# Kernel tuning notes

Measured on AMD Instinct MI355X. Metric: run time of the kernel, lower is better.

## Reference

```python
import jax, jax.numpy as jnp
import numpy as np
from jax import lax

STORAGE = 8
HIDDEN_HEAD = 32
N_BLOCKS = 16


def _conv(x, w, b, padding):
    # x: NCHW, w: OIHW
    y = lax.conv_general_dilated(
        x, w, window_strides=(1, 1), padding=padding,
        dimension_numbers=("NCHW", "OIHW", "NCHW"))
    return y + b[None, :, None, None]


def _min_pool3(x):
    # 3x3 sliding-window min, stride 1, same padding (pad value +inf so it
    return lax.reduce_window(x, float("inf"), lax.min,
                             (1, 1, 3, 3), (1, 1, 1, 1), "SAME")


def setup_inputs() -> dict:
    key = jax.random.key(0)
    ks = jax.random.split(key, 7)
    B, H, W = 8, 512, 512
    x = jax.random.normal(ks[0], (B, 1, H, W), dtype=jnp.float32)
    # initial 1x1 conv: 1 -> 8
    w0 = jax.random.normal(ks[1], (STORAGE, 1, 1, 1), dtype=jnp.float32) * 1.0
    b0 = jax.random.normal(ks[2], (STORAGE,), dtype=jnp.float32) * 0.1
    # head conv 3x3: 8 -> 32
    w1 = jax.random.normal(ks[3], (HIDDEN_HEAD, STORAGE, 3, 3), dtype=jnp.float32) * (1.0 / np.sqrt(STORAGE * 9))
    b1 = jax.random.normal(ks[4], (HIDDEN_HEAD,), dtype=jnp.float32) * 0.1
    # head conv 1x1: 32 -> 1
    w2 = jax.random.normal(ks[5], (1, HIDDEN_HEAD, 1, 1), dtype=jnp.float32) * (1.0 / np.sqrt(HIDDEN_HEAD))
    b2 = jax.random.normal(ks[6], (1,), dtype=jnp.float32) * 0.1
    return {"x": x, "w0": w0, "b0": b0, "w1": w1, "b1": b1, "w2": w2, "b2": b2}


def reference(x, w0, b0, w1, b1, w2, b2):
    h = _conv(x, w0, b0, "SAME")  # [B,8,H,W]
    for _ in range(N_BLOCKS):
        h = h + _min_pool3(h)
    h = _conv(h, w1, b1, "SAME")  # [B,32,H,W]
    h = jax.nn.relu(h)
    return _conv(h, w2, b2, "SAME")  # [B,1,H,W]
```

## Files before the change

### kernel.cpp

```cpp
#include <hip/hip_runtime.h>
#include <math.h>


#define N_PIX (512*512)
#define INF __builtin_inff()

typedef __attribute__((ext_vector_type(2))) float f2;

__device__ __forceinline__ float dpp_shr1(float v, float fill) {
    return __int_as_float(__builtin_amdgcn_update_dpp(
        __float_as_int(fill), __float_as_int(v), 0x138, 0xF, 0xF, false));
}
__device__ __forceinline__ float dpp_shl1(float v, float fill) {
    return __int_as_float(__builtin_amdgcn_update_dpp(
        __float_as_int(fill), __float_as_int(v), 0x130, 0xF, 0xF, false));
}
__device__ __forceinline__ float vmin3(float a, float b, float c) {
    float d;
    asm("v_min3_f32 %0, %1, %2, %3" : "=v"(d) : "v"(a), "v"(b), "v"(c));
    return d;
}

struct Row8 { float4 a, b; };

__device__ __forceinline__ Row8 row_update8(const Row8 up, const Row8 mid, const Row8 dn)
{
    float v0 = vmin3(up.a.x, mid.a.x, dn.a.x);
    float v1 = vmin3(up.a.y, mid.a.y, dn.a.y);
    float v2 = vmin3(up.a.z, mid.a.z, dn.a.z);
    float v3 = vmin3(up.a.w, mid.a.w, dn.a.w);
    float v4 = vmin3(up.b.x, mid.b.x, dn.b.x);
    float v5 = vmin3(up.b.y, mid.b.y, dn.b.y);
    float v6 = vmin3(up.b.z, mid.b.z, dn.b.z);
    float v7 = vmin3(up.b.w, mid.b.w, dn.b.w);
    float vmL = dpp_shr1(v7, INF);
    float vmR = dpp_shl1(v0, INF);
    Row8 o;
    o.a.x = mid.a.x + vmin3(vmL, v0, v1);
    o.a.y = mid.a.y + vmin3(v0, v1, v2);
    o.a.z = mid.a.z + vmin3(v1, v2, v3);
    o.a.w = mid.a.w + vmin3(v2, v3, v4);
    o.b.x = mid.b.x + vmin3(v3, v4, v5);
    o.b.y = mid.b.y + vmin3(v4, v5, v6);
    o.b.z = mid.b.z + vmin3(v5, v6, v7);
    o.b.w = mid.b.w + vmin3(v6, v7, vmR);
    return o;
}

__device__ __forceinline__ void halo_write(float* hp, const Row8& v) {
    hp[0*64]=v.a.x; hp[1*64]=v.a.y; hp[2*64]=v.a.z; hp[3*64]=v.a.w;
    hp[4*64]=v.b.x; hp[5*64]=v.b.y; hp[6*64]=v.b.z; hp[7*64]=v.b.w;
}
__device__ __forceinline__ Row8 halo_read(const float* hp) {
    Row8 v;
    v.a.x=hp[0*64]; v.a.y=hp[1*64]; v.a.z=hp[2*64]; v.a.w=hp[3*64];
    v.b.x=hp[4*64]; v.b.y=hp[5*64]; v.b.z=hp[6*64]; v.b.w=hp[7*64];
    return v;
}

__global__ __launch_bounds__(512, 2) void erode16_kernel(
    const float* __restrict__ x, float* __restrict__ A,
    const float* __restrict__ w0, const float* __restrict__ b0,
    const float* __restrict__ w1, const float* __restrict__ b1,
    float* __restrict__ W)
{
    if (blockIdx.x == 0 && blockIdx.y == 0 && threadIdx.x < 288) {
        int tid = threadIdx.x;
        int oc = tid / 9, k = tid - oc*9;
        float wp = 0.f, wq = 0.f;
        for (int ic = 0; ic < 8; ++ic) {
            float a = w0[ic];
            float w = w1[oc*72 + ic*9 + k];
            if (a > 0.f) wp += w * a;
            else         wq += w * (-a);
        }
        W[(oc*9 + k)*2 + 0] = wp;
        W[(oc*9 + k)*2 + 1] = wq;
        if (k == 0) {
            float beta[9];
            for (int kk = 0; kk < 9; ++kk) {
                float s = 0.f;
                for (int ic = 0; ic < 8; ++ic) s += b0[ic] * w1[oc*72 + ic*9 + kk];
                beta[kk] = 65536.0f * s;
            }
            float R[3], Lb[3], Rr[3];
            for (int r = 0; r < 3; ++r) {
                R[r]  = beta[r*3] + beta[r*3+1] + beta[r*3+2];
                Lb[r] = beta[r*3 + 0];
                Rr[r] = beta[r*3 + 2];
            }
            float bb = b1[oc];
            float Dv[3]  = { bb + R[1] + R[2], bb + R[0] + R[1] + R[2], bb + R[0] + R[1] };
            float ELv[3] = { Lb[1] + Lb[2], Lb[0] + Lb[1] + Lb[2], Lb[0] + Lb[1] };
            float ERv[3] = { Rr[1] + Rr[2], Rr[0] + Rr[1] + Rr[2], Rr[0] + Rr[1] };
            for (int c = 0; c < 3; ++c) {
                W[576 + (c*32 + oc)*2 + 0] = 0.5f * Dv[c];
                W[576 + (c*32 + oc)*2 + 1] = 0.5f * Dv[c];
                W[768 + c*32 + oc] = ELv[c];
                W[864 + c*32 + oc] = ERv[c];
            }
        }
    }

    __shared__ float halo[2][8][4][8][64];
    const int tid   = threadIdx.x;
    const int lane  = tid & 63;
    const int w     = tid >> 6;
    const int ty    = blockIdx.x;
    const int plane = blockIdx.y;
    const int colg  = lane * 8;
    const int row0g = ty*32 - 16 + w*8;

    const int wS = __builtin_amdgcn_readfirstlane(w);
    const bool edge_band = (wS == 0) || (wS == 7);

    const float* sp = x + (plane & 7)*N_PIX;
    const float sgn = (plane >= 8) ? -1.f : 1.f;

    Row8 h[8];
    #pragma unroll
    for (int r = 0; r < 8; ++r) {
        int gy = row0g + r;
        if ((unsigned)gy < 512u) {
            const float* rp = sp + gy*512 + colg;
            float4 a = *(const float4*)rp;
            float4 b = *(const float4*)(rp + 4);
            h[r].a = make_float4(a.x*sgn, a.y*sgn, a.z*sgn, a.w*sgn);
            h[r].b = make_float4(b.x*sgn, b.y*sgn, b.z*sgn, b.w*sgn);
        } else {
            h[r].a = make_float4(INF, INF, INF, INF);
            h[r].b = h[r].a;
        }
    }

    const Row8 inf8 = { make_float4(INF,INF,INF,INF), make_float4(INF,INF,INF,INF) };
    for (int s = 0; s < 8; ++s) {
        int par = s & 1;
        if (edge_band && s >= 4) { __syncthreads(); continue; }
        halo_write(&halo[par][w][0][0][lane], h[0]);
        halo_write(&halo[par][w][1][0][lane], h[1]);
        halo_write(&halo[par][w][2][0][lane], h[6]);
        halo_write(&halo[par][w][3][0][lane], h[7]);
        Row8 n2 = row_update8(h[1], h[2], h[3]);
        Row8 n3 = row_update8(h[2], h[3], h[4]);
        Row8 n4 = row_update8(h[3], h[4], h[5]);
        Row8 n5 = row_update8(h[4], h[5], h[6]);
        __syncthreads();
        Row8 um2 = inf8, um1 = inf8, dp0 = inf8, dp1 = inf8;
        if (w > 0) {
            um2 = halo_read(&halo[par][w-1][2][0][lane]);
            um1 = halo_read(&halo[par][w-1][3][0][lane]);
        }
        if (w < 7) {
            dp0 = halo_read(&halo[par][w+1][0][0][lane]);
            dp1 = halo_read(&halo[par][w+1][1][0][lane]);
        }
        Row8 nm1 = row_update8(um2, um1, h[0]);
        Row8 n0  = row_update8(um1, h[0], h[1]);
        Row8 n1  = row_update8(h[0], h[1], h[2]);
        Row8 n6  = row_update8(h[5], h[6], h[7]);
        Row8 n7  = row_update8(h[6], h[7], dp0);
        Row8 n8  = row_update8(h[7], dp0, dp1);
        h[0] = row_update8(nm1, n0, n1);
        h[1] = row_update8(n0,  n1, n2);
        h[2] = row_update8(n1,  n2, n3);
        h[3] = row_update8(n2,  n3, n4);
        h[4] = row_update8(n3,  n4, n5);
        h[5] = row_update8(n4,  n5, n6);
        h[6] = row_update8(n5,  n6, n7);
        h[7] = row_update8(n6,  n7, n8);
    }

    if (w >= 2 && w <= 5) {
        float* dp = A + plane*N_PIX;
        #pragma unroll
        for (int r = 0; r < 8; ++r) {
            float* op = dp + (row0g + r)*512 + colg;
            *(float4*)op       = h[r].a;
            *(float4*)(op + 4) = h[r].b;
        }
    }
}

__global__ __launch_bounds__(256) void head_kernel(
    const float* __restrict__ A, const float* __restrict__ W,
    const float* __restrict__ w2, const float* __restrict__ b2,
    float* __restrict__ out)
{
    const int tid  = threadIdx.x;
    const int lane = tid & 63;
    const int w    = tid >> 6;
    const int img  = blockIdx.x >> 7;
    const int y    = (blockIdx.x & 127)*4 + w;
    const int x0   = lane*8;

    const float* P = A + img*N_PIX;
    const float* Q = A + (8 + img)*N_PIX;

    f2 pq[3][10];
    #pragma unroll
    for (int dy = 0; dy < 3; ++dy) {
        int gy = y + dy - 1;
        if ((unsigned)gy < 512u) {
            const float* rp = P + gy*512 + x0;
            const float* rq = Q + gy*512 + x0;
            float4 a = *(const float4*)rp;
            float4 b = *(const float4*)(rp + 4);
            float4 c = *(const float4*)rq;
            float4 d = *(const float4*)(rq + 4);
            pq[dy][1] = (f2){a.x, c.x}; pq[dy][2] = (f2){a.y, c.y};
            pq[dy][3] = (f2){a.z, c.z}; pq[dy][4] = (f2){a.w, c.w};
            pq[dy][5] = (f2){b.x, d.x}; pq[dy][6] = (f2){b.y, d.y};
            pq[dy][7] = (f2){b.z, d.z}; pq[dy][8] = (f2){b.w, d.w};
            pq[dy][0] = (f2){dpp_shr1(b.w, 0.f), dpp_shr1(d.w, 0.f)};
            pq[dy][9] = (f2){dpp_shl1(a.x, 0.f), dpp_shl1(c.x, 0.f)};
        } else {
            #pragma unroll
            for (int j = 0; j < 10; ++j) pq[dy][j] = (f2){0.f, 0.f};
        }
    }

    const int wcase = (y == 0) ? 0 : ((y == 511) ? 2 : 1);
    const f2*    DH  = (const f2*)(W + 576);
    const float* ELt = W + 768 + wcase*32;
    const float* ERt = W + 864 + wcase*32;
    const float  mL  = (lane == 0)  ? -1.f : 0.f;
    const float  mR  = (lane == 63) ? -1.f : 0.f;

    float o[8];
    #pragma unroll
    for (int j = 0; j < 8; ++j) o[j] = 0.f;

    const f2* Wv = (const f2*)W;
    #pragma unroll 2
    for (int oc = 0; oc < 32; ++oc) {
        f2 acc[8];
        {
            f2 wv0 = Wv[oc*9];
            f2 hb  = DH[wcase*32 + oc];
            #pragma unroll
            for (int j = 0; j < 8; ++j) acc[j] = wv0 * pq[0][j] + hb;
        }
        #pragma unroll
        for (int t = 1; t < 9; ++t) {
            const int ky = t / 3, kx = t - ky*3;
            f2 wv = Wv[oc*9 + t];
            #pragma unroll
            for (int j = 0; j < 8; ++j) acc[j] += wv * pq[ky][kx + j];
        }
        float cl = ELt[oc];
        float cr = ERt[oc];
        float s[8];
        #pragma unroll
        for (int j = 0; j < 8; ++j) s[j] = acc[j].x + acc[j].y;
        s[0] = fmaf(cl, mL, s[0]);
        s[7] = fmaf(cr, mR, s[7]);
        float sc = w2[oc];
        #pragma unroll
        for (int j = 0; j < 8; ++j) o[j] += fmaxf(s[j], 0.f) * sc;
    }

    float bb = b2[0];
    float* op = out + img*N_PIX + y*512 + x0;
    *(float4*)(op)     = make_float4(o[0]+bb, o[1]+bb, o[2]+bb, o[3]+bb);
    *(float4*)(op + 4) = make_float4(o[4]+bb, o[5]+bb, o[6]+bb, o[7]+bb);
}

extern "C" void kernel_launch(void* const* d_in, const int* in_sizes, int n_in,
                              void* d_out, int out_size, void* d_ws, size_t ws_size,
                              hipStream_t stream) {
    const float* x  = (const float*)d_in[0];
    const float* w0 = (const float*)d_in[1];
    const float* b0 = (const float*)d_in[2];
    const float* w1 = (const float*)d_in[3];
    const float* b1 = (const float*)d_in[4];
    const float* w2 = (const float*)d_in[5];
    const float* b2 = (const float*)d_in[6];
    float* out = (float*)d_out;

    float* wsf = (float*)d_ws;
    float* A = wsf;
    float* W = wsf + 16*N_PIX;

    dim3 eg(16, 16);
    erode16_kernel<<<eg, 512, 0, stream>>>(x, A, w0, b0, w1, b1, W);

    head_kernel<<<1024, 256, 0, stream>>>(A, W, w2, b2, out);
}
```

Measured before the change: 122.7 us.

## Pack two output channels per pk_fma in head and vectorize swizzled LDS halo

The head conv is reorganized so each packed f32 lane holds two output channels rather than the P/Q halves of one channel. Weights are stored as scalar pairs and fed through inline v_pk_fma with op_sel, which removes the per-channel horizontal add and halves the epilogue relu/scale work. The erosion halo buffer moves from strided scalar LDS accesses to float4 accesses with an XOR swizzle to limit bank conflicts. The cost is more pk_fma issues, since the P and Q passes now run separately, and the use of inline asm with SGPR operands that the compiler must materialize.

Result: no change. 122.8 us (+0.1%).

```diff
diff --git a/kernel.cpp b/kernel.cpp
--- a/kernel.cpp
+++ b/kernel.cpp
@@ -6,6 +6,13 @@
 #define INF __builtin_inff()
 
 typedef __attribute__((ext_vector_type(2))) float f2;
+
+__device__ __forceinline__ unsigned long long f2bits(f2 v) {
+    union { f2 f; unsigned long long u; } c; c.f = v; return c.u;
+}
+__device__ __forceinline__ f2 bits2f(unsigned long long u) {
+    union { f2 f; unsigned long long u; } c; c.u = u; return c.f;
+}
 
 __device__ __forceinline__ float dpp_shr1(float v, float fill) {
     return __int_as_float(__builtin_amdgcn_update_dpp(
@@ -19,6 +26,25 @@
     float d;
     asm("v_min3_f32 %0, %1, %2, %3" : "=v"(d) : "v"(a), "v"(b), "v"(c));
     return d;
+}
+
+__device__ __forceinline__ void pkfma_P(f2& acc, unsigned long long w, f2 pq) {
+    unsigned long long a = f2bits(acc), p = f2bits(pq);
+    asm("v_pk_fma_f32 %0, %1, %2, %0 op_sel:[0,0,0] op_sel_hi:[1,0,1]"
+        : "+v"(a) : "s"(w), "v"(p));
+    acc = bits2f(a);
+}
+__device__ __forceinline__ void pkfma_Q(f2& acc, unsigned long long w, f2 pq) {
+    unsigned long long a = f2bits(acc), p = f2bits(pq);
+    asm("v_pk_fma_f32 %0, %1, %2, %0 op_sel:[0,1,0] op_sel_hi:[1,1,1]"
+        : "+v"(a) : "s"(w), "v"(p));
+    acc = bits2f(a);
+}
+__device__ __forceinline__ void pkmul_P(f2& acc, unsigned long long w, f2 pq) {
+    unsigned long long a, p = f2bits(pq);
+    asm("v_pk_mul_f32 %0, %1, %2 op_sel:[0,0] op_sel_hi:[1,0]"
+        : "=v"(a) : "s"(w), "v"(p));
+    acc = bits2f(a);
 }
 
 struct Row8 { float4 a, b; };
@@ -47,14 +73,14 @@
     return o;
 }
 
-__device__ __forceinline__ void halo_write(float* hp, const Row8& v) {
-    hp[0*64]=v.a.x; hp[1*64]=v.a.y; hp[2*64]=v.a.z; hp[3*64]=v.a.w;
-    hp[4*64]=v.b.x; hp[5*64]=v.b.y; hp[6*64]=v.b.z; hp[7*64]=v.b.w;
-}
-__device__ __forceinline__ Row8 halo_read(const float* hp) {
+__device__ __forceinline__ void halo_write(float* hp, int f0, int f1, const Row8& v) {
+    *(float4*)(hp + f0) = v.a;
+    *(float4*)(hp + f1) = v.b;
+}
+__device__ __forceinline__ Row8 halo_read(const float* hp, int f0, int f1) {
     Row8 v;
-    v.a.x=hp[0*64]; v.a.y=hp[1*64]; v.a.z=hp[2*64]; v.a.w=hp[3*64];
-    v.b.x=hp[4*64]; v.b.y=hp[5*64]; v.b.z=hp[6*64]; v.b.w=hp[7*64];
+    v.a = *(const float4*)(hp + f0);
+    v.b = *(const float4*)(hp + f1);
     return v;
 }
 
@@ -62,11 +88,12 @@
     const float* __restrict__ x, float* __restrict__ A,
     const float* __restrict__ w0, const float* __restrict__ b0,
     const float* __restrict__ w1, const float* __restrict__ b1,
-    float* __restrict__ W)
+    const float* __restrict__ w2, float* __restrict__ W)
 {
     if (blockIdx.x == 0 && blockIdx.y == 0 && threadIdx.x < 288) {
         int tid = threadIdx.x;
         int oc = tid / 9, k = tid - oc*9;
+        int o = oc >> 1, hf = oc & 1;
         float wp = 0.f, wq = 0.f;
         for (int ic = 0; ic < 8; ++ic) {
             float a = w0[ic];
@@ -74,8 +101,8 @@
             if (a > 0.f) wp += w * a;
             else         wq += w * (-a);
         }
-        W[(oc*9 + k)*2 + 0] = wp;
-        W[(oc*9 + k)*2 + 1] = wq;
+        W[(o*9 + k)*2 + hf]       = wp;
+        W[288 + (o*9 + k)*2 + hf] = wq;
         if (k == 0) {
             float beta[9];
             for (int kk = 0; kk < 9; ++kk) {
@@ -94,15 +121,15 @@
             float ELv[3] = { Lb[1] + Lb[2], Lb[0] + Lb[1] + Lb[2], Lb[0] + Lb[1] };
             float ERv[3] = { Rr[1] + Rr[2], Rr[0] + Rr[1] + Rr[2], Rr[0] + Rr[1] };
             for (int c = 0; c < 3; ++c) {
-                W[576 + (c*32 + oc)*2 + 0] = 0.5f * Dv[c];
-                W[576 + (c*32 + oc)*2 + 1] = 0.5f * Dv[c];
-                W[768 + c*32 + oc] = ELv[c];
-                W[864 + c*32 + oc] = ERv[c];
+                W[576 + c*32 + o*2 + hf] = Dv[c];
+                W[672 + c*32 + o*2 + hf] = ELv[c];
+                W[768 + c*32 + o*2 + hf] = ERv[c];
             }
-        }
-    }
-
-    __shared__ float halo[2][8][4][8][64];
+            W[864 + o*2 + hf] = w2[oc];
+        }
+    }
+
+    __shared__ float halo[2][8][4][512];
     const int tid   = threadIdx.x;
     const int lane  = tid & 63;
     const int w     = tid >> 6;
@@ -110,6 +137,9 @@
     const int plane = blockIdx.y;
     const int colg  = lane * 8;
     const int row0g = ty*32 - 16 + w*8;
+
+    const int f0 = (lane*8)     ^ (lane & 4);
+    const int f1 = (lane*8 + 4) ^ (lane & 4);
 
     const int wS = __builtin_amdgcn_readfirstlane(w);
     const bool edge_band = (wS == 0) || (wS == 7);
@@ -137,10 +167,10 @@
     for (int s = 0; s < 8; ++s) {
         int par = s & 1;
         if (edge_band && s >= 4) { __syncthreads(); continue; }
-        halo_write(&halo[par][w][0][0][lane], h[0]);
-        halo_write(&halo[par][w][1][0][lane], h[1]);
-        halo_write(&halo[par][w][2][0][lane], h[6]);
-        halo_write(&halo[par][w][3][0][lane], h[7]);
+        halo_write(&halo[par][w][0][0], f0, f1, h[0]);
+        halo_write(&halo[par][w][1][0], f0, f1, h[1]);
+        halo_write(&halo[par][w][2][0], f0, f1, h[6]);
+        halo_write(&halo[par][w][3][0], f0, f1, h[7]);
         Row8 n2 = row_update8(h[1], h[2], h[3]);
         Row8 n3 = row_update8(h[2], h[3], h[4]);
         Row8 n4 = row_update8(h[3], h[4], h[5]);
@@ -148,12 +178,12 @@
         __syncthreads();
         Row8 um2 = inf8, um1 = inf8, dp0 = inf8, dp1 = inf8;
         if (w > 0) {
-            um2 = halo_read(&halo[par][w-1][2][0][lane]);
-            um1 = halo_read(&halo[par][w-1][3][0][lane]);
+            um2 = halo_read(&halo[par][w-1][2][0], f0, f1);
+            um1 = halo_read(&halo[par][w-1][3][0], f0, f1);
         }
         if (w < 7) {
-            dp0 = halo_read(&halo[par][w+1][0][0][lane]);
-            dp1 = halo_read(&halo[par][w+1][1][0][lane]);
+            dp0 = halo_read(&halo[par][w+1][0][0], f0, f1);
+            dp1 = halo_read(&halo[par][w+1][1][0], f0, f1);
         }
         Row8 nm1 = row_update8(um2, um1, h[0]);
         Row8 n0  = row_update8(um1, h[0], h[1]);
@@ -184,8 +214,7 @@
 
 __global__ __launch_bounds__(256) void head_kernel(
     const float* __restrict__ A, const float* __restrict__ W,
-    const float* __restrict__ w2, const float* __restrict__ b2,
-    float* __restrict__ out)
+    const float* __restrict__ b2, float* __restrict__ out)
 {
     const int tid  = threadIdx.x;
     const int lane = tid & 63;
@@ -221,49 +250,65 @@
     }
 
     const int wcase = (y == 0) ? 0 : ((y == 511) ? 2 : 1);
-    const f2*    DH  = (const f2*)(W + 576);
-    const float* ELt = W + 768 + wcase*32;
-    const float* ERt = W + 864 + wcase*32;
-    const float  mL  = (lane == 0)  ? -1.f : 0.f;
-    const float  mR  = (lane == 63) ? -1.f : 0.f;
-
-    float o[8];
+    const unsigned long long* WPv = (const unsigned long long*)W;
+    const unsigned long long* WQv = (const unsigned long long*)(W + 288);
+    const f2* Dpv  = (const f2*)(W + 576 + wcase*32);
+    const f2* ELv  = (const f2*)(W + 672 + wcase*32);
+    const f2* ERv  = (const f2*)(W + 768 + wcase*32);
+    const f2* w2v  = (const f2*)(W + 864);
+    const float mLs = (lane == 0)  ? -1.f : 0.f;
+    const float mRs = (lane == 63) ? -1.f : 0.f;
+    const f2 mLp = (f2){mLs, mLs};
+    const f2 mRp = (f2){mRs, mRs};
+
+    f2 opk[8];
     #pragma unroll
-    for (int j = 0; j < 8; ++j) o[j] = 0.f;
-
-    const f2* Wv = (const f2*)W;
+    for (int j = 0; j < 8; ++j) opk[j] = (f2){0.f, 0.f};
+
     #pragma unroll 2
-    for (int oc = 0; oc < 32; ++oc) {
+    for (int o = 0; o < 16; ++o) {
         f2 acc[8];
         {
-            f2 wv0 = Wv[oc*9];
-            f2 hb  = DH[wcase*32 + oc];
+            unsigned long long wv = WPv[o*9];
             #pragma unroll
-            for (int j = 0; j < 8; ++j) acc[j] = wv0 * pq[0][j] + hb;
+            for (int j = 0; j < 8; ++j) pkmul_P(acc[j], wv, pq[0][j]);
         }
         #pragma unroll
         for (int t = 1; t < 9; ++t) {
             const int ky = t / 3, kx = t - ky*3;
-            f2 wv = Wv[oc*9 + t];
+            unsigned long long wv = WPv[o*9 + t];
             #pragma unroll
-            for (int j = 0; j < 8; ++j) acc[j] += wv * pq[ky][kx + j];
-        }
-        float cl = ELt[oc];
-        float cr = ERt[oc];
-        float s[8];
-        #pragma unroll
-        for (int j = 0; j < 8; ++j) s[j] = acc[j].x + acc[j].y;
-        s[0] = fmaf(cl, mL, s[0]);
-        s[7] = fmaf(cr, mR, s[7]);
-        float sc = w2[oc];
-        #pragma unroll
-        for (int j = 0; j < 8; ++j) o[j] += fmaxf(s[j], 0.f) * sc;
+            for (int j = 0; j < 8; ++j) pkfma_P(acc[j], wv, pq[ky][kx + j]);
+        }
+        #pragma unroll
+        for (int t = 0; t < 9; ++t) {
+            const int ky = t / 3, kx = t - ky*3;
+            unsigned long long wv = WQv[o*9 + t];
+            #pragma unroll
+            for (int j = 0; j < 8; ++j) pkfma_Q(acc[j], wv, pq[ky][kx + j]);
+        }
+        f2 bp = Dpv[o];
+        #pragma unroll
+        for (int j = 0; j < 8; ++j) acc[j] += bp;
+        acc[0] += ELv[o] * mLp;
+        acc[7] += ERv[o] * mRp;
+        f2 sc = w2v[o];
+        #pragma unroll
+        for (int j = 0; j < 8; ++j) {
+            acc[j].x = fmaxf(acc[j].x, 0.f);
+            acc[j].y = fmaxf(acc[j].y, 0.f);
+            opk[j] += acc[j] * sc;
+        }
     }
 
     float bb = b2[0];
+    float o0 = opk[0].x + opk[0].y + bb, o1 = opk[1].x + opk[1].y + bb;
+    float o2 = opk[2].x + opk[2].y + bb, o3 = opk[3].x + opk[3].y + bb;
+    float o4 = opk[4].x + opk[4].y + bb, o5 = opk[5].x + opk[5].y + bb;
+    float o6 = opk[6].x + opk[6].y + bb, o7 = opk[7].x + opk[7].y + bb;
     float* op = out + img*N_PIX + y*512 + x0;
-    *(float4*)(op)     = make_float4(o[0]+bb, o[1]+bb, o[2]+bb, o[3]+bb);
-    *(float4*)(op + 4) = make_float4(o[4]+bb, o[5]+bb, o[6]+bb, o[7]+bb);
+    *(float4*)(op)     = make_float4(o0, o1, o2, o3);
+    *(float4*)(op + 4) = make_float4(o4, o5, o6, o7);
 }
 
 extern "C" void kernel_launch(void* const* d_in, const int* in_sizes, int n_in,
@@ -283,7 +328,7 @@
     float* W = wsf + 16*N_PIX;
 
     dim3 eg(16, 16);
-    erode16_kernel<<<eg, 512, 0, stream>>>(x, A, w0, b0, w1, b1, W);
-
-    head_kernel<<<1024, 256, 0, stream>>>(A, W, w2, b2, out);
-}
+    erode16_kernel<<<eg, 512, 0, stream>>>(x, A, w0, b0, w1, b1, w2, W);
+
+    head_kernel<<<1024, 256, 0, stream>>>(A, W, b2, out);
+}
```
